# Performance work log

Measured on AMD Instinct MI355X. Metric: run time of the kernel, lower is better.

Reference implementation:

```python
import jax, jax.numpy as jnp
import numpy as np

D_MODEL = 512
NUM_HEADS = 8
HEAD_DIM = D_MODEL // NUM_HEADS
BATCH = 4
SEQ = 2048
NEG_INF = -1e9  # large negative instead of -inf so fully-masked rows stay finite


def setup_inputs() -> dict:
    key = jax.random.key(0)
    k1, k2, k3, k4 = jax.random.split(key, 4)
    x = jax.random.normal(k1, (BATCH, SEQ, D_MODEL), dtype=jnp.float32)
    mask = jnp.zeros((1, 1, SEQ, SEQ), dtype=jnp.float32)  # unused: paded_mask path taken
    paded_mask = jax.random.randint(k2, (BATCH, SEQ), 0, 2).astype(bool)
    W_qkv = jax.random.normal(k3, (D_MODEL, 3 * D_MODEL), dtype=jnp.float32) * (D_MODEL ** -0.5)
    W_out = jax.random.normal(k4, (D_MODEL, D_MODEL), dtype=jnp.float32) * (D_MODEL ** -0.5)
    return {"x": x, "mask": mask, "paded_mask": paded_mask, "W_qkv": W_qkv, "W_out": W_out}


def reference(x, mask, paded_mask, W_qkv, W_out):
    B, S, D = x.shape
    H, hd = NUM_HEADS, HEAD_DIM
    qkv = x @ W_qkv                                   # [B,S,3D]
    # Faithful to original: reshape (NOT transpose) (B,S,H,3hd) -> (B,H,S,3hd)
    qkv = qkv.reshape(B, S, H, 3 * hd).reshape(B, H, S, 3 * hd)
    q, k, v = jnp.split(qkv, 3, axis=3)               # each [B,H,S,hd]
    scaled = jnp.einsum("bhqd,bhkd->bhqk", q, k) / (hd ** 0.5)
    valid = paded_mask.astype(scaled.dtype)           # [B,S]
    # masked_padding_Decoder: softmax over valid keys for valid query rows,
    # zeros on invalid rows and invalid columns.
    logits = jnp.where(paded_mask[:, None, None, :], scaled, NEG_INF)
    att = jax.nn.softmax(logits, axis=-1)
    att = att * valid[:, None, :, None] * valid[:, None, None, :]
    values = jnp.einsum("bhqk,bhkd->bhqd", att, v)    # [B,H,S,hd]
    # Faithful to original: plain reshape (B,H,S,hd) -> (B,S,D)
    values = values.reshape(B, S, H * hd)
    return values @ W_out
```

## Files before the change

kernel.cpp:

```cpp
#include <hip/hip_runtime.h>
#include <hip/hip_bf16.h>
#include <math.h>
#include <stdint.h>

#define BATCH   4
#define SEQ     2048
#define DMODEL  512
#define NHEADS  8
#define HDIM    64
#define QKV_N   (3*DMODEL)

typedef short bf8  __attribute__((ext_vector_type(8)));
typedef float f32x4 __attribute__((ext_vector_type(4)));

#define MFMA16(a,b,c) __builtin_amdgcn_mfma_f32_16x16x32_bf16((a),(b),(c),0,0,0)

__device__ inline unsigned short f2bf(float f){
  unsigned int u = __float_as_uint(f);
  u += 0x7FFFu + ((u >> 16) & 1u);
  return (unsigned short)(u >> 16);
}

__device__ inline unsigned int pack_bf2(float a, float b){
  __hip_bfloat162 h = __float22bfloat162_rn(make_float2(a, b));
  return *reinterpret_cast<unsigned int*>(&h);
}

__device__ __forceinline__ float exp2_hw(float x){
#if defined(__has_builtin)
#if __has_builtin(__builtin_amdgcn_exp2f)
  return __builtin_amdgcn_exp2f(x);
#else
  float r; asm("v_exp_f32 %0, %1" : "=v"(r) : "v"(x)); return r;
#endif
#else
  float r; asm("v_exp_f32 %0, %1" : "=v"(r) : "v"(x)); return r;
#endif
}

__device__ __forceinline__ void gload_lds16(const unsigned short* g,
                                            unsigned short* l){
  __builtin_amdgcn_global_load_lds(
      (const __attribute__((address_space(1))) unsigned int*)g,
      (__attribute__((address_space(3))) unsigned int*)l,
      16, 0, 0);
}

__global__ __launch_bounds__(256) void prep(
    const float* __restrict__ x, const float* __restrict__ Wqkv,
    const float* __restrict__ Wout, const int* __restrict__ pmask,
    unsigned short* __restrict__ Xh, unsigned short* __restrict__ WqkvT,
    unsigned short* __restrict__ WoutT, int* __restrict__ Idx,
    int* __restrict__ Cnt)
{
  __shared__ unsigned short Ts[64][72];
  __shared__ int ps[256];
  __shared__ int tot;
  const int t = threadIdx.x;
  const int bx = blockIdx.x;
  if (bx < 2048) {
    const int i = bx*256 + t;
    const float4 a = reinterpret_cast<const float4*>(x)[2*i];
    const float4 b = reinterpret_cast<const float4*>(x)[2*i+1];
    uint4 o; unsigned short* us = reinterpret_cast<unsigned short*>(&o);
    us[0]=f2bf(a.x); us[1]=f2bf(a.y); us[2]=f2bf(a.z); us[3]=f2bf(a.w);
    us[4]=f2bf(b.x); us[5]=f2bf(b.y); us[6]=f2bf(b.z); us[7]=f2bf(b.w);
    reinterpret_cast<uint4*>(Xh)[i] = o;
    return;
  }
  if (bx >= 2304) {
    const int b = bx - 2304;
    const int* mb = pmask + b*SEQ;
    int loc[8]; int c = 0; const int base = t*8;
#pragma unroll
    for (int j=0;j<8;++j){ const int v = (mb[base+j] != 0); loc[j]=v; c+=v; }
    ps[t] = c; __syncthreads();
    for (int off=1; off<256; off<<=1){
      const int v = (t>=off) ? ps[t-off] : 0;
      __syncthreads(); ps[t] += v; __syncthreads();
    }
    int excl = ps[t] - c;
#pragma unroll
    for (int j=0;j<8;++j) if (loc[j]) Idx[b*SEQ + (excl++)] = base + j;
    if (t == 255){ Cnt[b] = ps[255]; tot = ps[255]; }
    __syncthreads();
    for (int k = tot + t; k < SEQ; k += 256) Idx[b*SEQ + k] = 0;
    return;
  }
  const float* in; unsigned short* out; int R, C, gx, gy;
  if (bx < 2048 + 192) {
    const int bid = bx - 2048;
    gx = bid % 24; gy = bid / 24; in = Wqkv; out = WqkvT; R = DMODEL; C = QKV_N;
  } else {
    const int bid = bx - 2240;
    gx = bid % 8;  gy = bid / 8;  in = Wout; out = WoutT; R = DMODEL; C = DMODEL;
  }
  const int r0 = gy<<6, c0 = gx<<6;
  const int rr = t>>2, cs = (t&3)<<4;
#pragma unroll
  for (int p=0;p<4;++p){
    float4 v = *reinterpret_cast<const float4*>(in + (size_t)(r0+rr)*C + c0 + cs + p*4);
    Ts[rr][cs+p*4+0]=f2bf(v.x); Ts[rr][cs+p*4+1]=f2bf(v.y);
    Ts[rr][cs+p*4+2]=f2bf(v.z); Ts[rr][cs+p*4+3]=f2bf(v.w);
  }
  __syncthreads();
  const int cc = t>>2, rs = (t&3)<<4;
#pragma unroll
  for (int p=0;p<4;++p){
    ushort4 o;
    o.x = Ts[rs+p*4+0][cc]; o.y = Ts[rs+p*4+1][cc];
    o.z = Ts[rs+p*4+2][cc]; o.w = Ts[rs+p*4+3][cc];
    *reinterpret_cast<ushort4*>(out + (size_t)(c0+cc)*R + r0 + rs + p*4) = o;
  }
}

__global__ __launch_bounds__(256) void gemm_qkv_mfma(
    const unsigned short* __restrict__ A, const unsigned short* __restrict__ Bt,
    unsigned short* __restrict__ QKV)
{
  __shared__ unsigned short As[128][64];
  __shared__ unsigned short Bs[128][64];
  const int t = threadIdx.x;
  const int w = t>>6, lane = t&63, quad = lane>>4, l15 = lane&15;
  const int wr = (w>>1)<<6, wc = (w&1)<<6;
  const int linear = blockIdx.y*12 + blockIdx.x;
  const int swz = (linear & 7)*96 + (linear >> 3);
  const int m0 = (swz/12)<<7, n0 = (swz%12)<<7;
  const int row = t>>3, seg = t&7;
  const unsigned short* Agp = A  + (size_t)(m0+row)*DMODEL + seg*8;
  const unsigned short* Bgp = Bt + (size_t)(n0+row)*DMODEL + seg*8;
  f32x4 acc[4][4];
#pragma unroll
  for (int i=0;i<4;++i)
#pragma unroll
    for (int j=0;j<4;++j) acc[i][j] = (f32x4){0.f,0.f,0.f,0.f};

  for (int k0=0;k0<DMODEL;k0+=64){
    __syncthreads();
#pragma unroll
    for (int p=0;p<4;++p){
      gload_lds16(Agp + (size_t)p*32*DMODEL + k0, &As[(w<<3)+(p<<5)][0]);
      gload_lds16(Bgp + (size_t)p*32*DMODEL + k0, &Bs[(w<<3)+(p<<5)][0]);
    }
    __syncthreads();
#pragma unroll
    for (int ks=0;ks<2;++ks){
      bf8 af[4], bfr[4];
#pragma unroll
      for (int mi=0;mi<4;++mi)
        af[mi]  = *reinterpret_cast<const bf8*>(&As[wr+mi*16+l15][ks*32+quad*8]);
#pragma unroll
      for (int nj=0;nj<4;++nj)
        bfr[nj] = *reinterpret_cast<const bf8*>(&Bs[wc+(l15<<2)+nj][ks*32+quad*8]);
#pragma unroll
      for (int mi=0;mi<4;++mi)
#pragma unroll
        for (int nj=0;nj<4;++nj) acc[mi][nj] = MFMA16(af[mi], bfr[nj], acc[mi][nj]);
    }
  }
  const int cbase = n0 + wc + (l15<<2);
  bool isq[4];
#pragma unroll
  for (int nj=0;nj<4;++nj) isq[nj] = ((cbase+nj) % 192) < 64;
#pragma unroll
  for (int mi=0;mi<4;++mi)
#pragma unroll
    for (int i=0;i<4;++i){
      const int m = m0 + wr + mi*16 + quad*4 + i;
      unsigned long long pk = 0;
#pragma unroll
      for (int nj=0;nj<4;++nj){
        float v = acc[mi][nj][i];
        if (isq[nj]) v *= 0.18033688f;
        pk |= (unsigned long long)f2bf(v) << (16*nj);
      }
      *reinterpret_cast<unsigned long long*>(QKV + (size_t)m*QKV_N + cbase) = pk;
    }
}

__global__ __launch_bounds__(256) void v_transpose(
    const unsigned short* __restrict__ QKV, const int* __restrict__ Idx,
    unsigned short* __restrict__ VT)
{
  __shared__ unsigned short Td[64][76];
  const int t = threadIdx.x;
  const int bh = blockIdx.y, b = bh>>3, hp = bh&7;
  const int s0 = blockIdx.x<<6;
  const size_t rbase = (size_t)(b*SEQ + hp*256);
  const int sr = t>>2, db = (t&3)<<4;
  const int s = Idx[b*SEQ + s0 + sr];
  const unsigned short* vp =
      QKV + (rbase + (s>>3))*QKV_N + (s&7)*192 + 128 + db;
  uint4 a = *reinterpret_cast<const uint4*>(vp);
  uint4 c = *reinterpret_cast<const uint4*>(vp + 8);
  const unsigned short* ua = reinterpret_cast<const unsigned short*>(&a);
  const unsigned short* uc = reinterpret_cast<const unsigned short*>(&c);
#pragma unroll
  for (int j=0;j<8;++j) Td[db+j][sr]   = ua[j];
#pragma unroll
  for (int j=0;j<8;++j) Td[db+8+j][sr] = uc[j];
  __syncthreads();
  const int L = t&15, d0 = t>>4;
  unsigned short* Op = VT + (size_t)bh*HDIM*SEQ + s0 + (L<<2);
#pragma unroll
  for (int cc=0;cc<4;++cc){
    const int d = d0 + (cc<<4);
    *reinterpret_cast<unsigned long long*>(Op + (size_t)d*SEQ) =
        *reinterpret_cast<const unsigned long long*>(&Td[d][L<<2]);
  }
}

__global__ __launch_bounds__(512, 4) void attn_mfma(
    const unsigned short* __restrict__ QKV, const unsigned short* __restrict__ VT,
    const int* __restrict__ mask, const int* __restrict__ Idx,
    const int* __restrict__ Cnt, unsigned short* __restrict__ O)
{
  __shared__ unsigned long long mbits[32];
  __shared__ unsigned short Ks[2][64][72];
  __shared__ unsigned short Vs[2][64][72];
  __shared__ unsigned short Pl[8][16][72];
  const int t = threadIdx.x;
  const int w = t>>6, lane = t&63, quad = lane>>4, l15 = lane&15;
  const int linear = blockIdx.y*16 + blockIdx.x;
  const int swz = (linear & 7)*64 + (linear >> 3);
  const int bh = swz >> 4, b = bh>>3, hp = bh&7;
  const int q0 = (swz & 15) << 7;
  const int qs = q0 + (w<<4);
  const int* mb = mask + b*SEQ;
  const f32x4 Z4 = {0.f,0.f,0.f,0.f};
#pragma unroll
  for (int i=0;i<4;++i){
    const unsigned long long bal = __ballot(mb[i*512 + t] != 0);
    if (lane == 0) mbits[i*8 + w] = bal;
  }
  const int kcnt = Cnt[b];
  const int kend = ((kcnt + 63) >> 6) << 6;
  const int* Idxb = Idx + b*SEQ;

  const size_t rbase = (size_t)(b*SEQ + hp*256);
  bf8 qf[2];
  {
    const int q = qs + l15;
    const unsigned short* qp =
        QKV + (rbase + (q>>3))*QKV_N + (q&7)*192 + (quad<<3);
    qf[0] = *reinterpret_cast<const bf8*>(qp);
    qf[1] = *reinterpret_cast<const bf8*>(qp + 32);
  }
  const unsigned short* Vg = VT + (size_t)bh*HDIM*SEQ;

  bf8 ones;
#pragma unroll
  for (int j=0;j<8;++j) ones[j] = (short)0x3F80;

  const int srow = t>>3, sc8 = (t&7)<<3;
  const int krow = ((srow&3)<<4) + (srow>>2);

  f32x4 of[4]; f32x4 lsv = Z4;
#pragma unroll
  for (int i=0;i<4;++i) of[i]=Z4;

  uint4 gk0, gv0;
  {
    const int s = Idxb[srow];
    const unsigned short* kp =
        QKV + (rbase + (s>>3))*QKV_N + (s&7)*192 + 64 + sc8;
    gk0 = *reinterpret_cast<const uint4*>(kp);
    gv0 = *reinterpret_cast<const uint4*>(Vg + (size_t)srow*SEQ + sc8);
  }
  *reinterpret_cast<uint4*>(&Ks[0][krow][sc8]) = gk0;
  *reinterpret_cast<uint4*>(&Vs[0][srow][sc8]) = gv0;
  {
    const int s = Idxb[64 + srow];
    const unsigned short* kp =
        QKV + (rbase + (s>>3))*QKV_N + (s&7)*192 + 64 + sc8;
    gk0 = *reinterpret_cast<const uint4*>(kp);
    gv0 = *reinterpret_cast<const uint4*>(Vg + (size_t)srow*SEQ + 64 + sc8);
  }
  __syncthreads();

  auto iter = [&](unsigned short (&KSC)[64][72], unsigned short (&VSC)[64][72],
                  unsigned short (&KSN)[64][72], unsigned short (&VSN)[64][72],
                  int kt) {
    if (kt + 64 < kend){
      *reinterpret_cast<uint4*>(&KSN[krow][sc8]) = gk0;
      *reinterpret_cast<uint4*>(&VSN[srow][sc8]) = gv0;
    }
    if (kt + 128 < kend){
      const int s = Idxb[kt + 128 + srow];
      const unsigned short* kp =
          QKV + (rbase + (s>>3))*QKV_N + (s&7)*192 + 64 + sc8;
      gk0 = *reinterpret_cast<const uint4*>(kp);
      gv0 = *reinterpret_cast<const uint4*>(
          Vg + (size_t)srow*SEQ + (kt + 128) + sc8);
    }

    bf8 kf[4][2];
#pragma unroll
    for (int nf=0;nf<4;++nf){
      kf[nf][0] = *reinterpret_cast<const bf8*>(&KSC[nf*16+l15][quad<<3]);
      kf[nf][1] = *reinterpret_cast<const bf8*>(&KSC[nf*16+l15][32+(quad<<3)]);
    }

    f32x4 sc[4];
    __builtin_amdgcn_s_setprio(1);
#pragma unroll
    for (int nf=0;nf<4;++nf){
      f32x4 s = MFMA16(qf[0], kf[nf][0], Z4);
      sc[nf] = MFMA16(qf[1], kf[nf][1], s);
    }
    __builtin_amdgcn_s_setprio(0);
    const int kbase = kt + (l15<<2);
    float pv[4][4];
#pragma unroll
    for (int nf=0;nf<4;++nf){
      const bool on = (kbase + nf) < kcnt;
#pragma unroll
      for (int i=0;i<4;++i)
        pv[nf][i] = on ? exp2_hw(sc[nf][i]) : 0.f;
    }
#pragma unroll
    for (int i=0;i<4;++i){
      const unsigned int lo = pack_bf2(pv[0][i], pv[1][i]);
      const unsigned int hi = pack_bf2(pv[2][i], pv[3][i]);
      *reinterpret_cast<unsigned long long*>(&Pl[w][(quad<<2)+i][l15<<2]) =
          ((unsigned long long)hi<<32) | lo;
    }

    bf8 pa[2];
    pa[0] = *reinterpret_cast<const bf8*>(&Pl[w][l15][quad<<3]);
    pa[1] = *reinterpret_cast<const bf8*>(&Pl[w][l15][32+(quad<<3)]);
    __builtin_amdgcn_s_setprio(1);
    {
      f32x4 l = MFMA16(pa[0], ones, lsv);
      lsv = MFMA16(pa[1], ones, l);
    }
#pragma unroll
    for (int nf=0;nf<4;++nf){
      const bf8 v0 = *reinterpret_cast<const bf8*>(&VSC[nf*16+l15][quad<<3]);
      const bf8 v1 = *reinterpret_cast<const bf8*>(&VSC[nf*16+l15][32+(quad<<3)]);
      f32x4 o = MFMA16(pa[0], v0, of[nf]);
      of[nf] = MFMA16(pa[1], v1, o);
    }
    __builtin_amdgcn_s_setprio(0);
    __syncthreads();
  };

  for (int kt=0; kt<kend; kt+=128){
    iter(Ks[0], Vs[0], Ks[1], Vs[1], kt);
    if (kt + 64 < kend)
      iter(Ks[1], Vs[1], Ks[0], Vs[0], kt+64);
  }

  unsigned short* Op = O + (size_t)bh*SEQ*HDIM;
  const unsigned long long qw = mbits[qs >> 6];
#pragma unroll
  for (int i=0;i<4;++i){
    const int q = qs + (quad<<2) + i;
    const bool qv = (qw >> (q & 63)) & 1ull;
    const float l = lsv[i];
    const float inv = (qv && l > 0.f) ? 1.f/l : 0.f;
#pragma unroll
    for (int nf=0;nf<4;++nf)
      Op[(size_t)q*HDIM + (nf<<4) + l15] = f2bf(of[nf][i]*inv);
  }
}

__global__ __launch_bounds__(256) void gemm_out_mfma(
    const unsigned short* __restrict__ A, const unsigned short* __restrict__ Bt,
    float* __restrict__ Out)
{
  __shared__ unsigned short As[128][64];
  __shared__ unsigned short Bs[64][64];
  const int t = threadIdx.x;
  const int w = t>>6, lane = t&63, quad = lane>>4, l15 = lane&15;
  const int wr = (w>>1)<<6, wc = (w&1)<<5;
  const int linear = blockIdx.y*8 + blockIdx.x;
  const int swz = (linear & 7)*64 + (linear >> 3);
  const int m0 = (swz>>3)<<7, n0 = (swz&7)<<6;
  const int row = t>>3, seg = t&7;
  const unsigned short* Agp = A  + (size_t)(m0+row)*DMODEL + seg*8;
  const unsigned short* Bgp = Bt + (size_t)(n0+row)*DMODEL + seg*8;
  f32x4 acc[4][2];
#pragma unroll
  for (int i=0;i<4;++i)
#pragma unroll
    for (int j=0;j<2;++j) acc[i][j] = (f32x4){0.f,0.f,0.f,0.f};

  for (int k0=0;k0<DMODEL;k0+=64){
    __syncthreads();
#pragma unroll
    for (int p=0;p<4;++p)
      gload_lds16(Agp + (size_t)p*32*DMODEL + k0, &As[(w<<3)+(p<<5)][0]);
#pragma unroll
    for (int p=0;p<2;++p)
      gload_lds16(Bgp + (size_t)p*32*DMODEL + k0, &Bs[(w<<3)+(p<<5)][0]);
    __syncthreads();
#pragma unroll
    for (int ks=0;ks<2;++ks){
      bf8 af[4], bfr[2];
#pragma unroll
      for (int mi=0;mi<4;++mi)
        af[mi]  = *reinterpret_cast<const bf8*>(&As[wr+mi*16+l15][ks*32+quad*8]);
#pragma unroll
      for (int nj=0;nj<2;++nj)
        bfr[nj] = *reinterpret_cast<const bf8*>(&Bs[wc+(l15<<1)+nj][ks*32+quad*8]);
#pragma unroll
      for (int mi=0;mi<4;++mi)
#pragma unroll
        for (int nj=0;nj<2;++nj) acc[mi][nj] = MFMA16(af[mi], bfr[nj], acc[mi][nj]);
    }
  }
  const int cbase = n0 + wc + (l15<<1);
#pragma unroll
  for (int mi=0;mi<4;++mi)
#pragma unroll
    for (int i=0;i<4;++i){
      const int m = m0 + wr + mi*16 + quad*4 + i;
      const float2 o = make_float2(acc[mi][0][i], acc[mi][1][i]);
      *reinterpret_cast<float2*>(Out + (size_t)m*DMODEL + cbase) = o;
    }
}

extern "C" void kernel_launch(void* const* d_in, const int* in_sizes, int n_in,
                              void* d_out, int out_size, void* d_ws, size_t ws_size,
                              hipStream_t stream) {
  (void)in_sizes; (void)n_in; (void)out_size; (void)ws_size;
  const float* x     = (const float*)d_in[0];
  const int*   pmask = (const int*)d_in[2];
  const float* Wqkv  = (const float*)d_in[3];
  const float* Wout  = (const float*)d_in[4];
  float* out = (float*)d_out;

  const size_t per = (size_t)BATCH*NHEADS*SEQ*HDIM;
  unsigned short* Xh    = (unsigned short*)d_ws;
  unsigned short* WqkvT = Xh    + (size_t)8192*512;
  unsigned short* WoutT = WqkvT + (size_t)1536*512;
  unsigned short* QKVb  = WoutT + (size_t)512*512;
  unsigned short* VbT   = QKVb  + (size_t)8192*QKV_N;
  unsigned short* Ob    = VbT + per;
  int* Idx = (int*)(Ob + per);
  int* Cnt = Idx + (size_t)BATCH*SEQ;

  prep<<<2308, 256, 0, stream>>>(x, Wqkv, Wout, pmask, Xh, WqkvT, WoutT,
                                 Idx, Cnt);
  gemm_qkv_mfma<<<dim3(QKV_N/128, 8192/128), 256, 0, stream>>>(Xh, WqkvT, QKVb);
  v_transpose<<<dim3(SEQ/64, BATCH*NHEADS), 256, 0, stream>>>(QKVb, Idx, VbT);
  attn_mfma<<<dim3(SEQ/128, BATCH*NHEADS), 512, 0, stream>>>(
      QKVb, VbT, pmask, Idx, Cnt, Ob);
  gemm_out_mfma<<<dim3(DMODEL/64, 8192/128), 256, 0, stream>>>(Ob, WoutT, out);
}
```

Measured before the change: 170.8 us.

## Compact query rows to valid tokens and skip padded attention work

Attention now iterates only over valid (compacted) query rows gathered through the index list, and scatters outputs back to their original positions. Blocks whose query range lies beyond the valid count exit early. The output buffer is zeroed in the prep kernel so that invalid rows stay zero. v_transpose also skips tiles past the valid count, and attention blocks shrink from 512 to 256 threads with 64-query tiles. This is intended to roughly halve the attention work for masks with about 50% valid tokens, at the cost of an extra zero-fill pass over the output buffer and scattered output writes.

```diff
diff --git a/kernel.cpp b/kernel.cpp
--- a/kernel.cpp
+++ b/kernel.cpp
@@ -51,7 +51,7 @@
     const float* __restrict__ Wout, const int* __restrict__ pmask,
     unsigned short* __restrict__ Xh, unsigned short* __restrict__ WqkvT,
     unsigned short* __restrict__ WoutT, int* __restrict__ Idx,
-    int* __restrict__ Cnt)
+    int* __restrict__ Cnt, unsigned short* __restrict__ Ob)
 {
   __shared__ unsigned short Ts[64][72];
   __shared__ int ps[256];
@@ -66,6 +66,13 @@
     us[0]=f2bf(a.x); us[1]=f2bf(a.y); us[2]=f2bf(a.z); us[3]=f2bf(a.w);
     us[4]=f2bf(b.x); us[5]=f2bf(b.y); us[6]=f2bf(b.z); us[7]=f2bf(b.w);
     reinterpret_cast<uint4*>(Xh)[i] = o;
+    return;
+  }
+  if (bx >= 2308) {
+    const int g = (bx - 2308)*256 + t;
+    uint4 z = {0u,0u,0u,0u};
+    uint4* p = reinterpret_cast<uint4*>(Ob) + (size_t)g*4;
+    p[0]=z; p[1]=z; p[2]=z; p[3]=z;
     return;
   }
   if (bx >= 2304) {
@@ -180,12 +187,13 @@
 
 __global__ __launch_bounds__(256) void v_transpose(
     const unsigned short* __restrict__ QKV, const int* __restrict__ Idx,
-    unsigned short* __restrict__ VT)
+    const int* __restrict__ Cnt, unsigned short* __restrict__ VT)
 {
   __shared__ unsigned short Td[64][76];
   const int t = threadIdx.x;
   const int bh = blockIdx.y, b = bh>>3, hp = bh&7;
   const int s0 = blockIdx.x<<6;
+  if (s0 >= ((Cnt[b] + 63) & ~63)) return;
   const size_t rbase = (size_t)(b*SEQ + hp*256);
   const int sr = t>>2, db = (t&3)<<4;
   const int s = Idx[b*SEQ + s0 + sr];
@@ -210,39 +218,33 @@
   }
 }
 
-__global__ __launch_bounds__(512, 4) void attn_mfma(
+__global__ __launch_bounds__(256, 4) void attn_mfma(
     const unsigned short* __restrict__ QKV, const unsigned short* __restrict__ VT,
-    const int* __restrict__ mask, const int* __restrict__ Idx,
-    const int* __restrict__ Cnt, unsigned short* __restrict__ O)
+    const int* __restrict__ Idx, const int* __restrict__ Cnt,
+    unsigned short* __restrict__ O)
 {
-  __shared__ unsigned long long mbits[32];
   __shared__ unsigned short Ks[2][64][72];
   __shared__ unsigned short Vs[2][64][72];
-  __shared__ unsigned short Pl[8][16][72];
+  __shared__ unsigned short Pl[4][16][72];
   const int t = threadIdx.x;
   const int w = t>>6, lane = t&63, quad = lane>>4, l15 = lane&15;
-  const int linear = blockIdx.y*16 + blockIdx.x;
-  const int swz = (linear & 7)*64 + (linear >> 3);
-  const int bh = swz >> 4, b = bh>>3, hp = bh&7;
-  const int q0 = (swz & 15) << 7;
+  const int linear = blockIdx.y*32 + blockIdx.x;
+  const int swz = (linear & 7)*128 + (linear >> 3);
+  const int bh = swz >> 5, b = bh>>3, hp = bh&7;
+  const int q0 = (swz & 31) << 6;
+  const int kcnt = Cnt[b];
+  const int kend = (kcnt + 63) & ~63;
+  if (q0 >= kend) return;
   const int qs = q0 + (w<<4);
-  const int* mb = mask + b*SEQ;
+  const int* Idxb = Idx + b*SEQ;
   const f32x4 Z4 = {0.f,0.f,0.f,0.f};
-#pragma unroll
-  for (int i=0;i<4;++i){
-    const unsigned long long bal = __ballot(mb[i*512 + t] != 0);
-    if (lane == 0) mbits[i*8 + w] = bal;
-  }
-  const int kcnt = Cnt[b];
-  const int kend = ((kcnt + 63) >> 6) << 6;
-  const int* Idxb = Idx + b*SEQ;
 
   const size_t rbase = (size_t)(b*SEQ + hp*256);
   bf8 qf[2];
   {
-    const int q = qs + l15;
+    const int sq = Idxb[qs + l15];
     const unsigned short* qp =
-        QKV + (rbase + (q>>3))*QKV_N + (q&7)*192 + (quad<<3);
+        QKV + (rbase + (sq>>3))*QKV_N + (sq&7)*192 + (quad<<3);
     qf[0] = *reinterpret_cast<const bf8*>(qp);
     qf[1] = *reinterpret_cast<const bf8*>(qp + 32);
   }
@@ -252,29 +254,37 @@
 #pragma unroll
   for (int j=0;j<8;++j) ones[j] = (short)0x3F80;
 
-  const int srow = t>>3, sc8 = (t&7)<<3;
+  const int srow = t>>2, sc4 = (t&3)<<4;
   const int krow = ((srow&3)<<4) + (srow>>2);
 
   f32x4 of[4]; f32x4 lsv = Z4;
 #pragma unroll
   for (int i=0;i<4;++i) of[i]=Z4;
 
-  uint4 gk0, gv0;
+  uint4 gk0, gk1, gv0, gv1;
   {
     const int s = Idxb[srow];
     const unsigned short* kp =
-        QKV + (rbase + (s>>3))*QKV_N + (s&7)*192 + 64 + sc8;
+        QKV + (rbase + (s>>3))*QKV_N + (s&7)*192 + 64 + sc4;
     gk0 = *reinterpret_cast<const uint4*>(kp);
-    gv0 = *reinterpret_cast<const uint4*>(Vg + (size_t)srow*SEQ + sc8);
-  }
-  *reinterpret_cast<uint4*>(&Ks[0][krow][sc8]) = gk0;
-  *reinterpret_cast<uint4*>(&Vs[0][srow][sc8]) = gv0;
+    gk1 = *reinterpret_cast<const uint4*>(kp + 8);
+    const unsigned short* vp = Vg + (size_t)srow*SEQ + sc4;
+    gv0 = *reinterpret_cast<const uint4*>(vp);
+    gv1 = *reinterpret_cast<const uint4*>(vp + 8);
+  }
+  *reinterpret_cast<uint4*>(&Ks[0][krow][sc4])   = gk0;
+  *reinterpret_cast<uint4*>(&Ks[0][krow][sc4+8]) = gk1;
+  *reinterpret_cast<uint4*>(&Vs[0][srow][sc4])   = gv0;
+  *reinterpret_cast<uint4*>(&Vs[0][srow][sc4+8]) = gv1;
   {
     const int s = Idxb[64 + srow];
     const unsigned short* kp =
-        QKV + (rbase + (s>>3))*QKV_N + (s&7)*192 + 64 + sc8;
+        QKV + (rbase + (s>>3))*QKV_N + (s&7)*192 + 64 + sc4;
     gk0 = *reinterpret_cast<const uint4*>(kp);
-    gv0 = *reinterpret_cast<const uint4*>(Vg + (size_t)srow*SEQ + 64 + sc8);
+    gk1 = *reinterpret_cast<const uint4*>(kp + 8);
+    const unsigned short* vp = Vg + (size_t)srow*SEQ + 64 + sc4;
+    gv0 = *reinterpret_cast<const uint4*>(vp);
+    gv1 = *reinterpret_cast<const uint4*>(vp + 8);
   }
   __syncthreads();
 
@@ -282,16 +292,20 @@
                   unsigned short (&KSN)[64][72], unsigned short (&VSN)[64][72],
                   int kt) {
     if (kt + 64 < kend){
-      *reinterpret_cast<uint4*>(&KSN[krow][sc8]) = gk0;
-      *reinterpret_cast<uint4*>(&VSN[srow][sc8]) = gv0;
+      *reinterpret_cast<uint4*>(&KSN[krow][sc4])   = gk0;
+      *reinterpret_cast<uint4*>(&KSN[krow][sc4+8]) = gk1;
+      *reinterpret_cast<uint4*>(&VSN[srow][sc4])   = gv0;
+      *reinterpret_cast<uint4*>(&VSN[srow][sc4+8]) = gv1;
     }
     if (kt + 128 < kend){
       const int s = Idxb[kt + 128 + srow];
       const unsigned short* kp =
-          QKV + (rbase + (s>>3))*QKV_N + (s&7)*192 + 64 + sc8;
+          QKV + (rbase + (s>>3))*QKV_N + (s&7)*192 + 64 + sc4;
       gk0 = *reinterpret_cast<const uint4*>(kp);
-      gv0 = *reinterpret_cast<const uint4*>(
-          Vg + (size_t)srow*SEQ + (kt + 128) + sc8);
+      gk1 = *reinterpret_cast<const uint4*>(kp + 8);
+      const unsigned short* vp = Vg + (size_t)srow*SEQ + (kt + 128) + sc4;
+      gv0 = *reinterpret_cast<const uint4*>(vp);
+      gv1 = *reinterpret_cast<const uint4*>(vp + 8);
     }
 
     bf8 kf[4][2];
@@ -352,16 +366,17 @@
   }
 
   unsigned short* Op = O + (size_t)bh*SEQ*HDIM;
-  const unsigned long long qw = mbits[qs >> 6];
 #pragma unroll
   for (int i=0;i<4;++i){
     const int q = qs + (quad<<2) + i;
-    const bool qv = (qw >> (q & 63)) & 1ull;
-    const float l = lsv[i];
-    const float inv = (qv && l > 0.f) ? 1.f/l : 0.f;
-#pragma unroll
-    for (int nf=0;nf<4;++nf)
-      Op[(size_t)q*HDIM + (nf<<4) + l15] = f2bf(of[nf][i]*inv);
+    if (q < kcnt){
+      const int orig = Idxb[q];
+      const float l = lsv[i];
+      const float inv = (l > 0.f) ? 1.f/l : 0.f;
+#pragma unroll
+      for (int nf=0;nf<4;++nf)
+        Op[(size_t)orig*HDIM + (nf<<4) + l15] = f2bf(of[nf][i]*inv);
+    }
   }
 }
 
@@ -441,11 +456,12 @@
   int* Idx = (int*)(Ob + per);
   int* Cnt = Idx + (size_t)BATCH*SEQ;
 
-  prep<<<2308, 256, 0, stream>>>(x, Wqkv, Wout, pmask, Xh, WqkvT, WoutT,
-                                 Idx, Cnt);
+  prep<<<2820, 256, 0, stream>>>(x, Wqkv, Wout, pmask, Xh, WqkvT, WoutT,
+                                 Idx, Cnt, Ob);
   gemm_qkv_mfma<<<dim3(QKV_N/128, 8192/128), 256, 0, stream>>>(Xh, WqkvT, QKVb);
-  v_transpose<<<dim3(SEQ/64, BATCH*NHEADS), 256, 0, stream>>>(QKVb, Idx, VbT);
-  attn_mfma<<<dim3(SEQ/128, BATCH*NHEADS), 512, 0, stream>>>(
-      QKVb, VbT, pmask, Idx, Cnt, Ob);
+  v_transpose<<<dim3(SEQ/64, BATCH*NHEADS), 256, 0, stream>>>(
+      QKVb, Idx, Cnt, VbT);
+  attn_mfma<<<dim3(SEQ/64, BATCH*NHEADS), 256, 0, stream>>>(
+      QKVb, VbT, Idx, Cnt, Ob);
   gemm_out_mfma<<<dim3(DMODEL/64, 8192/128), 256, 0, stream>>>(Ob, WoutT, out);
 }
```

New measurement: 168.4 us. Within noise of the previous version (-1.5%).

## Compact query rows to valid positions and skip padded query blocks in attention

Applied to the files above, without the earlier changes.

Attention now gathers only valid query rows through the compacted index list and exits early for query blocks beyond the valid count. Outputs are scattered back to their original positions, and invalid rows are zero-filled by extra prep blocks that clear the output buffer. The V transpose also skips blocks beyond the valid key count. This roughly halves attention work for random masks, at the cost of a zeroing pass over the output and scattered writes.

```diff
diff --git a/kernel.cpp b/kernel.cpp
--- a/kernel.cpp
+++ b/kernel.cpp
@@ -51,7 +51,7 @@
     const float* __restrict__ Wout, const int* __restrict__ pmask,
     unsigned short* __restrict__ Xh, unsigned short* __restrict__ WqkvT,
     unsigned short* __restrict__ WoutT, int* __restrict__ Idx,
-    int* __restrict__ Cnt)
+    int* __restrict__ Cnt, unsigned short* __restrict__ Ob)
 {
   __shared__ unsigned short Ts[64][72];
   __shared__ int ps[256];
@@ -66,6 +66,13 @@
     us[0]=f2bf(a.x); us[1]=f2bf(a.y); us[2]=f2bf(a.z); us[3]=f2bf(a.w);
     us[4]=f2bf(b.x); us[5]=f2bf(b.y); us[6]=f2bf(b.z); us[7]=f2bf(b.w);
     reinterpret_cast<uint4*>(Xh)[i] = o;
+    return;
+  }
+  if (bx >= 2308) {
+    const int g = (bx - 2308)*256 + t;
+    uint4 z = {0u,0u,0u,0u};
+    uint4* p = reinterpret_cast<uint4*>(Ob) + (size_t)g*4;
+    p[0]=z; p[1]=z; p[2]=z; p[3]=z;
     return;
   }
   if (bx >= 2304) {
@@ -180,12 +187,13 @@
 
 __global__ __launch_bounds__(256) void v_transpose(
     const unsigned short* __restrict__ QKV, const int* __restrict__ Idx,
-    unsigned short* __restrict__ VT)
+    const int* __restrict__ Cnt, unsigned short* __restrict__ VT)
 {
   __shared__ unsigned short Td[64][76];
   const int t = threadIdx.x;
   const int bh = blockIdx.y, b = bh>>3, hp = bh&7;
   const int s0 = blockIdx.x<<6;
+  if (s0 >= ((Cnt[b] + 63) & ~63)) return;
   const size_t rbase = (size_t)(b*SEQ + hp*256);
   const int sr = t>>2, db = (t&3)<<4;
   const int s = Idx[b*SEQ + s0 + sr];
@@ -212,10 +220,9 @@
 
 __global__ __launch_bounds__(512, 4) void attn_mfma(
     const unsigned short* __restrict__ QKV, const unsigned short* __restrict__ VT,
-    const int* __restrict__ mask, const int* __restrict__ Idx,
-    const int* __restrict__ Cnt, unsigned short* __restrict__ O)
+    const int* __restrict__ Idx, const int* __restrict__ Cnt,
+    unsigned short* __restrict__ O)
 {
-  __shared__ unsigned long long mbits[32];
   __shared__ unsigned short Ks[2][64][72];
   __shared__ unsigned short Vs[2][64][72];
   __shared__ unsigned short Pl[8][16][72];
@@ -225,24 +232,19 @@
   const int swz = (linear & 7)*64 + (linear >> 3);
   const int bh = swz >> 4, b = bh>>3, hp = bh&7;
   const int q0 = (swz & 15) << 7;
+  const int kcnt = Cnt[b];
+  const int kend = (kcnt + 63) & ~63;
+  if (q0 >= kend) return;
   const int qs = q0 + (w<<4);
-  const int* mb = mask + b*SEQ;
+  const int* Idxb = Idx + b*SEQ;
   const f32x4 Z4 = {0.f,0.f,0.f,0.f};
-#pragma unroll
-  for (int i=0;i<4;++i){
-    const unsigned long long bal = __ballot(mb[i*512 + t] != 0);
-    if (lane == 0) mbits[i*8 + w] = bal;
-  }
-  const int kcnt = Cnt[b];
-  const int kend = ((kcnt + 63) >> 6) << 6;
-  const int* Idxb = Idx + b*SEQ;
 
   const size_t rbase = (size_t)(b*SEQ + hp*256);
   bf8 qf[2];
   {
-    const int q = qs + l15;
+    const int sq = Idxb[qs + l15];
     const unsigned short* qp =
-        QKV + (rbase + (q>>3))*QKV_N + (q&7)*192 + (quad<<3);
+        QKV + (rbase + (sq>>3))*QKV_N + (sq&7)*192 + (quad<<3);
     qf[0] = *reinterpret_cast<const bf8*>(qp);
     qf[1] = *reinterpret_cast<const bf8*>(qp + 32);
   }
@@ -352,16 +354,17 @@
   }
 
   unsigned short* Op = O + (size_t)bh*SEQ*HDIM;
-  const unsigned long long qw = mbits[qs >> 6];
 #pragma unroll
   for (int i=0;i<4;++i){
     const int q = qs + (quad<<2) + i;
-    const bool qv = (qw >> (q & 63)) & 1ull;
-    const float l = lsv[i];
-    const float inv = (qv && l > 0.f) ? 1.f/l : 0.f;
-#pragma unroll
-    for (int nf=0;nf<4;++nf)
-      Op[(size_t)q*HDIM + (nf<<4) + l15] = f2bf(of[nf][i]*inv);
+    if (q < kcnt){
+      const int orig = Idxb[q];
+      const float l = lsv[i];
+      const float inv = (l > 0.f) ? 1.f/l : 0.f;
+#pragma unroll
+      for (int nf=0;nf<4;++nf)
+        Op[(size_t)orig*HDIM + (nf<<4) + l15] = f2bf(of[nf][i]*inv);
+    }
   }
 }
 
@@ -441,11 +444,12 @@
   int* Idx = (int*)(Ob + per);
   int* Cnt = Idx + (size_t)BATCH*SEQ;
 
-  prep<<<2308, 256, 0, stream>>>(x, Wqkv, Wout, pmask, Xh, WqkvT, WoutT,
-                                 Idx, Cnt);
+  prep<<<2820, 256, 0, stream>>>(x, Wqkv, Wout, pmask, Xh, WqkvT, WoutT,
+                                 Idx, Cnt, Ob);
   gemm_qkv_mfma<<<dim3(QKV_N/128, 8192/128), 256, 0, stream>>>(Xh, WqkvT, QKVb);
-  v_transpose<<<dim3(SEQ/64, BATCH*NHEADS), 256, 0, stream>>>(QKVb, Idx, VbT);
+  v_transpose<<<dim3(SEQ/64, BATCH*NHEADS), 256, 0, stream>>>(
+      QKVb, Idx, Cnt, VbT);
   attn_mfma<<<dim3(SEQ/128, BATCH*NHEADS), 512, 0, stream>>>(
-      QKVb, VbT, pmask, Idx, Cnt, Ob);
+      QKVb, VbT, Idx, Cnt, Ob);
   gemm_out_mfma<<<dim3(DMODEL/64, 8192/128), 256, 0, stream>>>(Ob, WoutT, out);
 }
```

After: 170.2 us. Within noise of the previous version (-0.4%).
